# Kernel tuning notes

Measured on AMD Instinct MI355X. Metric: run time of the kernel, lower is better.

The kernel has to match this reference:

```python
import jax, jax.numpy as jnp
import numpy as np

V, E, H, L, B = 50000, 300, 128, 32, 8


def setup_inputs() -> dict:
    key = jax.random.key(0)
    ks = jax.random.split(key, 12)
    s = 0.05
    d = {}
    d["premise"] = jax.random.randint(ks[0], (B, L), 0, V)
    d["hypothesis"] = jax.random.randint(ks[1], (B, L), 0, V)
    d["emb"] = jax.random.normal(ks[2], (V, E), jnp.float32) * s
    d["W_ih"] = jax.random.normal(ks[3], (8 * H, 2 * E), jnp.float32) * s
    d["b_ih"] = jnp.zeros((8 * H,), jnp.float32)
    d["W_hh"] = jax.random.normal(ks[4], (8 * H, 2 * H), jnp.float32) * s
    d["b_hh"] = jnp.zeros((8 * H,), jnp.float32)
    d["W_ch"] = jax.random.normal(ks[5], (H, 2 * H), jnp.float32) * s
    d["b_ch"] = jnp.zeros((H,), jnp.float32)
    d["W_cc"] = jax.random.normal(ks[6], (H, 2 * H), jnp.float32) * s
    d["b_cc"] = jnp.zeros((H,), jnp.float32)
    d["W1"] = jax.random.normal(ks[7], (H, H), jnp.float32) * s
    d["b1"] = jnp.zeros((H,), jnp.float32)
    d["W2"] = jax.random.normal(ks[8], (H, H), jnp.float32) * s
    d["b2"] = jnp.zeros((H,), jnp.float32)
    d["W3"] = jax.random.normal(ks[9], (3, H), jnp.float32) * s
    d["b3"] = jnp.zeros((3,), jnp.float32)
    return d


def _lstm_cell(x, h, c, W_ih, b_ih, W_hh, b_hh):
    # PyTorch LSTMCell gate order: i, f, g, o
    g = x @ W_ih.T + b_ih + h @ W_hh.T + b_hh
    i, f, gg, o = jnp.split(g, 4, axis=-1)
    c_new = jax.nn.sigmoid(f) * c + jax.nn.sigmoid(i) * jnp.tanh(gg)
    h_new = jax.nn.sigmoid(o) * jnp.tanh(c_new)
    return h_new, c_new


def reference(premise, hypothesis, emb, W_ih, b_ih, W_hh, b_hh,
              W_ch, b_ch, W_cc, b_cc, W1, b1, W2, b2, W3, b3):
    p = emb[premise]      # [B, L, E]
    hyp = emb[hypothesis]  # [B, L, E]
    Bn, Ln, En = p.shape
    Hn = W_ch.shape[0]
    p_t = jnp.swapaxes(p, 0, 1)    # [L, B, E]
    hyp_t = jnp.swapaxes(hyp, 0, 1)
    z = jnp.zeros((Bn, Hn), p.dtype)

    def row_step(row_carry, p_i):
        h_up, c_up = row_carry  # [L, B, H] from previous row (left deps)

        def col_step(carry, xs):
            h_low, c_low = carry       # [B, H] from previous column (lower deps)
            h_u, c_u, x_hyp = xs       # [B,H], [B,H], [B,E]
            x = jnp.concatenate([p_i, x_hyp], axis=-1)       # [B, 2E]
            h_in = jnp.concatenate([h_u, h_low], axis=-1)    # left then lower -> [B, 2H]
            c_in = jnp.concatenate([c_u, c_low], axis=-1)
            h_o, c_o = _lstm_cell(x, h_in, c_in, W_ih, b_ih, W_hh, b_hh)
            h_n = h_o @ W_ch.T + b_ch  # condense back to [B, H]
            c_n = c_o @ W_cc.T + b_cc
            return (h_n, c_n), (h_n, c_n)

        _, (h_row, c_row) = jax.lax.scan(col_step, (z, z), (h_up, c_up, hyp_t))
        return (h_row, c_row), None

    init = (jnp.zeros((Ln, Bn, Hn), p.dtype), jnp.zeros((Ln, Bn, Hn), p.dtype))
    (h_grid, _), _ = jax.lax.scan(row_step, init, p_t)
    h = h_grid[-1]  # h[L, L] corner state, [B, H]
    h = jax.nn.relu(h @ W1.T + b1)
    h = jax.nn.relu(h @ W2.T + b2)
    return jax.nn.softmax(h @ W3.T + b3, axis=1)
```

## Files before the change

### kernel.cpp

```cpp
#include <hip/hip_runtime.h>
#include <math.h>


typedef _Float16 h2 __attribute__((ext_vector_type(2)));

__device__ __forceinline__ h2 pk_f16(float a, float b) {
    return __builtin_bit_cast(h2, __builtin_amdgcn_cvt_pkrtz(a, b));
}

#define HYP_OFF   0
#define HO_OFF    262144
#define CO_OFF    524288
#define WP_OFF    786432
#define B_OFF     1048576
#define FLAGS_OFF 1050624

#define BASE 0xAAAAAAAAu

__device__ __forceinline__ float sigm(float x) { return 1.f / (1.f + __expf(-x)); }
__device__ __forceinline__ float tanh_fast(float x) { return 1.f - 2.f / (__expf(2.f * x) + 1.f); }

__device__ __forceinline__ unsigned ld_flag(const unsigned* p) {
    return __hip_atomic_load(p, __ATOMIC_RELAXED, __HIP_MEMORY_SCOPE_AGENT);
}
__device__ __forceinline__ void st_flag(unsigned* p, unsigned v) {
    __hip_atomic_store(p, v, __ATOMIC_RELAXED, __HIP_MEMORY_SCOPE_AGENT);
}
__device__ __forceinline__ float ld_f32(const float* p) {
    unsigned u = __hip_atomic_load((const unsigned*)p, __ATOMIC_RELAXED, __HIP_MEMORY_SCOPE_AGENT);
    return __uint_as_float(u);
}
__device__ __forceinline__ void st_f32(float* p, float v) {
    __hip_atomic_store((unsigned*)p, __float_as_uint(v), __ATOMIC_RELAXED, __HIP_MEMORY_SCOPE_AGENT);
}
__device__ __forceinline__ void st_u32(unsigned* p, unsigned v) {
    __hip_atomic_store(p, v, __ATOMIC_RELAXED, __HIP_MEMORY_SCOPE_AGENT);
}
__device__ __forceinline__ float2 ld_f32x2(const float* p) {
    unsigned long long u = __hip_atomic_load((const unsigned long long*)p,
                                             __ATOMIC_RELAXED, __HIP_MEMORY_SCOPE_AGENT);
    float2 r; r.x = __uint_as_float((unsigned)u); r.y = __uint_as_float((unsigned)(u >> 32));
    return r;
}
__device__ __forceinline__ void ld_u32x2(const unsigned* p, unsigned& a, unsigned& b) {
    unsigned long long u = __hip_atomic_load((const unsigned long long*)p,
                                             __ATOMIC_RELAXED, __HIP_MEMORY_SCOPE_AGENT);
    a = (unsigned)u; b = (unsigned)(u >> 32);
}
__device__ __forceinline__ void wait_ge(const unsigned* f, unsigned target) {
    long spins = 0;
    while ((ld_flag(f) - BASE) < target) {
        __builtin_amdgcn_s_sleep(1);
        if (++spins > (1L << 22)) break;
    }
}
__device__ __forceinline__ void drain_vmem() {
    asm volatile("s_waitcnt vmcnt(0)" ::: "memory");
}

__global__ void __launch_bounds__(256, 1) grid_lstm_kernel(
    const int* __restrict__ premise, const int* __restrict__ hypothesis,
    const float* __restrict__ emb,
    const float* __restrict__ W_ih, const float* __restrict__ b_ih,
    const float* __restrict__ W_hh, const float* __restrict__ b_hh,
    const float* __restrict__ W_ch, const float* __restrict__ b_ch,
    const float* __restrict__ W_cc, const float* __restrict__ b_cc,
    const float* __restrict__ W1, const float* __restrict__ b1,
    const float* __restrict__ W2, const float* __restrict__ b2,
    const float* __restrict__ W3, const float* __restrict__ b3,
    float* __restrict__ out, float* __restrict__ ws)
{
    __shared__ h2    hAB[2048];
    __shared__ float sCo[2048];
    __shared__ float ppL[1024];
    __shared__ float red[8448];
    __shared__ float red2[2304];

    const int tid = threadIdx.x;
    const int bid = blockIdx.x;
    const int i   = bid & 31;
    const int c   = bid >> 5;

    float*    Hypproj = ws + HYP_OFF;
    float*    Ho      = ws + HO_OFF;
    float*    Co      = ws + CO_OFF;
    unsigned* WP      = (unsigned*)(ws + WP_OFF);
    float*    BU      = ws + B_OFF;
    float*    BL      = ws + B_OFF + 1024;
    unsigned* HF      = (unsigned*)(ws + FLAGS_OFF);
    unsigned* InitF   = (unsigned*)(ws + FLAGS_OFF) + 4096;

    const int tq = tid & 31, ks = tid >> 5;
    const int tl = tid & 31, bb = tid >> 5;

    {
        float* embs = red;
        for (int idx = tid; idx < 4800; idx += 256) {
            int side = idx / 2400, rem = idx - side * 2400;
            int b = rem / 300, e = rem - b * 300;
            const int* toks = side ? hypothesis : premise;
            embs[idx] = emb[(long)toks[b * 32 + i] * 300 + e];
        }
        __syncthreads();
        #pragma unroll 1
        for (int q = 0; q < 4; q++) {
            const int oo = tid + q * 256;
            const int b = oo >> 7, g = oo & 127;
            const int gr = (g >> 5) * 256 + c * 32 + (g & 31);
            float accP = b_ih[gr] + b_hh[gr];
            float accH = 0.f;
            const float* wp = W_ih + (long)gr * 600;
            const float* eP = embs + b * 300;
            const float* eH = embs + 2400 + b * 300;
            for (int e = 0; e < 300; e += 4) {
                float4 w1 = *(const float4*)(wp + e);
                float4 w2v = *(const float4*)(wp + 300 + e);
                float4 p4 = *(const float4*)(eP + e);
                float4 h4 = *(const float4*)(eH + e);
                accP += w1.x * p4.x + w1.y * p4.y + w1.z * p4.z + w1.w * p4.w;
                accH += w2v.x * h4.x + w2v.y * h4.y + w2v.z * h4.z + w2v.w * h4.w;
            }
            st_f32(&Hypproj[i * 8192 + b * 1024 + gr], accH);
            ppL[b * 128 + g] = accP;
        }
        __syncthreads();
    }

    {
        const int tr = tid >> 6, col = (tid & 63) * 4;
        const int r  = bid * 4 + tr;
        float u[4] = {0.f, 0.f, 0.f, 0.f}, l[4] = {0.f, 0.f, 0.f, 0.f};
        const float* whU = W_hh + (long)r * 256;
        const float* whL = whU + 128;
        for (int k = 0; k < 128; k++) {
            const float wu = whU[k], wl = whL[k];
            float4 wc = *(const float4*)(W_ch + (long)k * 256 + col);
            u[0] += wu * wc.x; u[1] += wu * wc.y; u[2] += wu * wc.z; u[3] += wu * wc.w;
            l[0] += wl * wc.x; l[1] += wl * wc.y; l[2] += wl * wc.z; l[3] += wl * wc.w;
        }
        unsigned* wrow = WP + (long)r * 256;
        st_u32(&wrow[col / 2],       __builtin_bit_cast(unsigned, __builtin_amdgcn_cvt_pkrtz(u[0], u[1])));
        st_u32(&wrow[col / 2 + 1],   __builtin_bit_cast(unsigned, __builtin_amdgcn_cvt_pkrtz(u[2], u[3])));
        st_u32(&wrow[128 + col / 2],     __builtin_bit_cast(unsigned, __builtin_amdgcn_cvt_pkrtz(l[0], l[1])));
        st_u32(&wrow[128 + col / 2 + 1], __builtin_bit_cast(unsigned, __builtin_amdgcn_cvt_pkrtz(l[2], l[3])));
        if ((tid & 63) == 0) {
            float su = 0.f, sl = 0.f;
            for (int k = 0; k < 128; k++) { su += whU[k] * b_ch[k]; sl += whL[k] * b_ch[k]; }
            st_f32(&BU[r], su); st_f32(&BL[r], sl);
        }
    }
    drain_vmem();
    __syncthreads();
    if (tid == 0) st_flag(&InitF[bid * 16], BASE + 1u);

    wait_ge(&InitF[tid * 16], 1u);
    __syncthreads();

    h2 w[4][32];
    #pragma unroll
    for (int a = 0; a < 4; a++) {
        const unsigned* src = WP + (long)(a * 256 + c * 32 + tq) * 256 + ks * 32;
        #pragma unroll
        for (int m = 0; m < 16; m++) {
            unsigned lo, hi;
            ld_u32x2(src + m * 2, lo, hi);
            w[a][2 * m]     = __builtin_bit_cast(h2, lo);
            w[a][2 * m + 1] = __builtin_bit_cast(h2, hi);
        }
    }
    float4 w3[8];
    {
        const float* wr = W_cc + (long)((c & 3) * 32 + tq) * 256 + ks * 32;
        #pragma unroll
        for (int m = 0; m < 8; m++) w3[m] = *(const float4*)(wr + m * 4);
    }
    float bUv[4], bLv[4];
    #pragma unroll
    for (int a = 0; a < 4; a++) {
        bUv[a] = ld_f32(&BU[a * 256 + c * 32 + tl]);
        bLv[a] = ld_f32(&BL[a * 256 + c * 32 + tl]);
    }

    #pragma unroll 1
    for (int j = 0; j < 32; j++) {
        const bool upok = (i > 0), lfok = (j > 0);
        const bool cok  = (c < 4) ? upok : lfok;
        const int  jl   = lfok ? (j - 1) : 0;

        if (upok && tid < 8)              wait_ge(&HF[((i - 1) * 8 + tid) * 16], (unsigned)(j + 1));
        if (lfok && tid >= 8 && tid < 16) wait_ge(&HF[(i * 8 + (tid - 8)) * 16], (unsigned)j);
        __syncthreads();

        float hyv[4];
        #pragma unroll
        for (int a = 0; a < 4; a++)
            hyv[a] = ld_f32(&Hypproj[j * 8192 + bb * 1024 + a * 256 + c * 32 + tl]);

        const float* HoUp = Ho + ((((i - 1) & 3) * 32 + j) * 2048);
        const float* HoLf = Ho + (((i & 3) * 32 + jl) * 2048);
        const float* CoS  = (c < 4) ? Co + ((((i - 1) & 3) * 32 + j) * 2048)
                                    : Co + (((i & 3) * 32 + jl) * 2048);
        #pragma unroll
        for (int r = 0; r < 4; r++) {
            const int idx = r * 256 + tid;
            const int b = idx >> 7, kk = idx & 127;
            float2 u = upok ? ld_f32x2(HoUp + b * 256 + 2 * kk) : make_float2(0.f, 0.f);
            float2 l = lfok ? ld_f32x2(HoLf + b * 256 + 2 * kk) : make_float2(0.f, 0.f);
            float2 cv = cok ? ld_f32x2(CoS + b * 256 + 2 * kk) : make_float2(0.f, 0.f);
            hAB[b * 256 + kk]       = pk_f16(u.x, u.y);
            hAB[b * 256 + 128 + kk] = pk_f16(l.x, l.y);
            sCo[b * 256 + 2 * kk] = cv.x; sCo[b * 256 + 2 * kk + 1] = cv.y;
        }
        __syncthreads();

        float acc[4][8], a3[8];
        #pragma unroll
        for (int a = 0; a < 4; a++)
            #pragma unroll
            for (int b = 0; b < 8; b++) acc[a][b] = 0.f;
        #pragma unroll
        for (int b = 0; b < 8; b++) a3[b] = 0.f;
        #pragma unroll
        for (int b = 0; b < 8; b++) {
            const h2*    hb = hAB + b * 256 + ks * 32;
            const float* cb = sCo + b * 256 + ks * 32;
            #pragma unroll
            for (int m4 = 0; m4 < 8; m4++) {
                uint4 hu = *(const uint4*)(hb + m4 * 4);
                h2 h0 = __builtin_bit_cast(h2, hu.x);
                h2 h1 = __builtin_bit_cast(h2, hu.y);
                h2 h2v = __builtin_bit_cast(h2, hu.z);
                h2 h3 = __builtin_bit_cast(h2, hu.w);
                #pragma unroll
                for (int a = 0; a < 4; a++) {
                    acc[a][b] = __builtin_amdgcn_fdot2(w[a][m4 * 4],     h0,  acc[a][b], false);
                    acc[a][b] = __builtin_amdgcn_fdot2(w[a][m4 * 4 + 1], h1,  acc[a][b], false);
                    acc[a][b] = __builtin_amdgcn_fdot2(w[a][m4 * 4 + 2], h2v, acc[a][b], false);
                    acc[a][b] = __builtin_amdgcn_fdot2(w[a][m4 * 4 + 3], h3,  acc[a][b], false);
                }
                float4 cv = *(const float4*)(cb + m4 * 4);
                a3[b] += w3[m4].x * cv.x + w3[m4].y * cv.y + w3[m4].z * cv.z + w3[m4].w * cv.w;
            }
        }
        #pragma unroll
        for (int a = 0; a < 4; a++)
            #pragma unroll
            for (int b = 0; b < 8; b++) red[tid * 33 + a * 8 + b] = acc[a][b];
        #pragma unroll
        for (int b = 0; b < 8; b++) red2[tid * 9 + b] = a3[b];
        __syncthreads();

        {
            float g4[4];
            #pragma unroll
            for (int a = 0; a < 4; a++) {
                float s = 0.f;
                #pragma unroll
                for (int k = 0; k < 8; k++)
                    s += red[(k * 32 + tl) * 33 + a * 8 + bb];
                s += ppL[bb * 128 + a * 32 + tl] + hyv[a];
                if (upok) s += bUv[a];
                if (lfok) s += bLv[a];
                g4[a] = s;
            }
            float ci = 0.f;
            #pragma unroll
            for (int k = 0; k < 8; k++) ci += red2[(k * 32 + tl) * 9 + bb];
            if (cok) ci += b_cc[(c & 3) * 32 + tl];
            const float cnew = sigm(g4[1]) * ci + sigm(g4[0]) * tanh_fast(g4[2]);
            const float hnew = sigm(g4[3]) * tanh_fast(cnew);
            const int base = ((i & 3) * 32 + j) * 2048 + bb * 256 + c * 32 + tl;
            st_f32(&Ho[base], hnew);
            st_f32(&Co[base], cnew);
        }
        drain_vmem();
        __syncthreads();
        if (tid == 0) st_flag(&HF[(i * 8 + c) * 16], BASE + (unsigned)(j + 1));
    }

    if (bid == 31) {
        if (tid < 8) wait_ge(&HF[(31 * 8 + tid) * 16], 32u);
        __syncthreads();
        const float* HoF = Ho + (((31 & 3) * 32 + 31) * 2048);
        #pragma unroll
        for (int r = 0; r < 4; r++) {
            const int idx = r * 256 + tid;
            float2 v = ld_f32x2(HoF + idx * 2);
            sCo[idx * 2] = v.x; sCo[idx * 2 + 1] = v.y;
        }
        __syncthreads();
        #pragma unroll 1
        for (int q = 0; q < 4; q++) {
            const int oo = tid + q * 256;
            const int b = oo >> 7, o = oo & 127;
            float a = b_ch[o];
            const float* wr = W_ch + (long)o * 256;
            const float* x = sCo + b * 256;
            for (int k = 0; k < 256; k += 4) {
                float4 wv = *(const float4*)(wr + k);
                float4 xv = *(const float4*)(x + k);
                a += wv.x * xv.x + wv.y * xv.y + wv.z * xv.z + wv.w * xv.w;
            }
            ppL[b * 128 + o] = a;
        }
        __syncthreads();
        float* m1 = red;
        float* m2 = red + 1024;
        for (int idx = tid; idx < 1024; idx += 256) {
            int b = idx >> 7, o = idx & 127;
            float a = b1[o];
            const float* wr = W1 + o * 128; const float* x = ppL + b * 128;
            for (int k = 0; k < 128; k++) a += wr[k] * x[k];
            m1[idx] = fmaxf(a, 0.f);
        }
        __syncthreads();
        for (int idx = tid; idx < 1024; idx += 256) {
            int b = idx >> 7, o = idx & 127;
            float a = b2[o];
            const float* wr = W2 + o * 128; const float* x = m1 + b * 128;
            for (int k = 0; k < 128; k++) a += wr[k] * x[k];
            m2[idx] = fmaxf(a, 0.f);
        }
        __syncthreads();
        if (tid < 8) {
            const int b = tid;
            float lg[3];
            for (int cc = 0; cc < 3; cc++) {
                float a = b3[cc];
                const float* wr = W3 + cc * 128; const float* x = m2 + b * 128;
                for (int k = 0; k < 128; k++) a += wr[k] * x[k];
                lg[cc] = a;
            }
            float m = fmaxf(lg[0], fmaxf(lg[1], lg[2]));
            float e0 = expf(lg[0] - m), e1 = expf(lg[1] - m), e2 = expf(lg[2] - m);
            float s = e0 + e1 + e2;
            out[b * 3 + 0] = e0 / s;
            out[b * 3 + 1] = e1 / s;
            out[b * 3 + 2] = e2 / s;
        }
    }
}

extern "C" void kernel_launch(void* const* d_in, const int* in_sizes, int n_in,
                              void* d_out, int out_size, void* d_ws, size_t ws_size,
                              hipStream_t stream) {
    const int*   premise    = (const int*)d_in[0];
    const int*   hypothesis = (const int*)d_in[1];
    const float* emb        = (const float*)d_in[2];
    const float* W_ih       = (const float*)d_in[3];
    const float* b_ih       = (const float*)d_in[4];
    const float* W_hh       = (const float*)d_in[5];
    const float* b_hh       = (const float*)d_in[6];
    const float* W_ch       = (const float*)d_in[7];
    const float* b_ch       = (const float*)d_in[8];
    const float* W_cc       = (const float*)d_in[9];
    const float* b_cc       = (const float*)d_in[10];
    const float* W1         = (const float*)d_in[11];
    const float* b1         = (const float*)d_in[12];
    const float* W2         = (const float*)d_in[13];
    const float* b2         = (const float*)d_in[14];
    const float* W3         = (const float*)d_in[15];
    const float* b3         = (const float*)d_in[16];
    float* out = (float*)d_out;
    float* ws  = (float*)d_ws;

    (void)in_sizes; (void)n_in; (void)out_size; (void)ws_size;

    grid_lstm_kernel<<<dim3(256), dim3(256), 0, stream>>>(
        premise, hypothesis, emb, W_ih, b_ih, W_hh, b_hh,
        W_ch, b_ch, W_cc, b_cc, W1, b1, W2, b2, W3, b3, out, ws);
}
```

Baseline: 815.9 us.

## Split recurrent matvec so left-dependency half runs before waiting on upper row

The per-step wait on both the upper-row and left-column flags is split into two phases. The block first waits only on its own row's previous column, loads the left h/c state and computes the left half of the recurrent dot products. Only then does it wait for the upper row's flag and compute the upper half. This overlaps computation with the cross-block dependency wait in the wavefront. It adds an extra barrier and reshuffles the weight register layout.

```diff
diff --git a/kernel.cpp b/kernel.cpp
--- a/kernel.cpp
+++ b/kernel.cpp
@@ -156,16 +156,20 @@
     wait_ge(&InitF[tid * 16], 1u);
     __syncthreads();
 
-    h2 w[4][32];
+    h2 w_u[4][16], w_l[4][16];
     #pragma unroll
     for (int a = 0; a < 4; a++) {
-        const unsigned* src = WP + (long)(a * 256 + c * 32 + tq) * 256 + ks * 32;
-        #pragma unroll
-        for (int m = 0; m < 16; m++) {
+        const unsigned* srcU = WP + (long)(a * 256 + c * 32 + tq) * 256 + ks * 16;
+        const unsigned* srcL = srcU + 128;
+        #pragma unroll
+        for (int m = 0; m < 8; m++) {
             unsigned lo, hi;
-            ld_u32x2(src + m * 2, lo, hi);
-            w[a][2 * m]     = __builtin_bit_cast(h2, lo);
-            w[a][2 * m + 1] = __builtin_bit_cast(h2, hi);
+            ld_u32x2(srcU + m * 2, lo, hi);
+            w_u[a][2 * m]     = __builtin_bit_cast(h2, lo);
+            w_u[a][2 * m + 1] = __builtin_bit_cast(h2, hi);
+            ld_u32x2(srcL + m * 2, lo, hi);
+            w_l[a][2 * m]     = __builtin_bit_cast(h2, lo);
+            w_l[a][2 * m + 1] = __builtin_bit_cast(h2, hi);
         }
     }
     float4 w3[8];
@@ -187,8 +191,7 @@
         const bool cok  = (c < 4) ? upok : lfok;
         const int  jl   = lfok ? (j - 1) : 0;
 
-        if (upok && tid < 8)              wait_ge(&HF[((i - 1) * 8 + tid) * 16], (unsigned)(j + 1));
-        if (lfok && tid >= 8 && tid < 16) wait_ge(&HF[(i * 8 + (tid - 8)) * 16], (unsigned)j);
+        if (lfok && tid < 8) wait_ge(&HF[(i * 8 + tid) * 16], (unsigned)j);
         __syncthreads();
 
         float hyv[4];
@@ -196,20 +199,18 @@
         for (int a = 0; a < 4; a++)
             hyv[a] = ld_f32(&Hypproj[j * 8192 + bb * 1024 + a * 256 + c * 32 + tl]);
 
-        const float* HoUp = Ho + ((((i - 1) & 3) * 32 + j) * 2048);
         const float* HoLf = Ho + (((i & 3) * 32 + jl) * 2048);
-        const float* CoS  = (c < 4) ? Co + ((((i - 1) & 3) * 32 + j) * 2048)
-                                    : Co + (((i & 3) * 32 + jl) * 2048);
+        const float* CoLf = Co + (((i & 3) * 32 + jl) * 2048);
         #pragma unroll
         for (int r = 0; r < 4; r++) {
             const int idx = r * 256 + tid;
             const int b = idx >> 7, kk = idx & 127;
-            float2 u = upok ? ld_f32x2(HoUp + b * 256 + 2 * kk) : make_float2(0.f, 0.f);
             float2 l = lfok ? ld_f32x2(HoLf + b * 256 + 2 * kk) : make_float2(0.f, 0.f);
-            float2 cv = cok ? ld_f32x2(CoS + b * 256 + 2 * kk) : make_float2(0.f, 0.f);
-            hAB[b * 256 + kk]       = pk_f16(u.x, u.y);
             hAB[b * 256 + 128 + kk] = pk_f16(l.x, l.y);
-            sCo[b * 256 + 2 * kk] = cv.x; sCo[b * 256 + 2 * kk + 1] = cv.y;
+            if (c >= 4) {
+                float2 cv = lfok ? ld_f32x2(CoLf + b * 256 + 2 * kk) : make_float2(0.f, 0.f);
+                sCo[b * 256 + 2 * kk] = cv.x; sCo[b * 256 + 2 * kk + 1] = cv.y;
+            }
         }
         __syncthreads();
 
@@ -222,10 +223,9 @@
         for (int b = 0; b < 8; b++) a3[b] = 0.f;
         #pragma unroll
         for (int b = 0; b < 8; b++) {
-            const h2*    hb = hAB + b * 256 + ks * 32;
-            const float* cb = sCo + b * 256 + ks * 32;
-            #pragma unroll
-            for (int m4 = 0; m4 < 8; m4++) {
+            const h2* hb = hAB + b * 256 + 128 + ks * 16;
+            #pragma unroll
+            for (int m4 = 0; m4 < 4; m4++) {
                 uint4 hu = *(const uint4*)(hb + m4 * 4);
                 h2 h0 = __builtin_bit_cast(h2, hu.x);
                 h2 h1 = __builtin_bit_cast(h2, hu.y);
@@ -233,13 +233,65 @@
                 h2 h3 = __builtin_bit_cast(h2, hu.w);
                 #pragma unroll
                 for (int a = 0; a < 4; a++) {
-                    acc[a][b] = __builtin_amdgcn_fdot2(w[a][m4 * 4],     h0,  acc[a][b], false);
-                    acc[a][b] = __builtin_amdgcn_fdot2(w[a][m4 * 4 + 1], h1,  acc[a][b], false);
-                    acc[a][b] = __builtin_amdgcn_fdot2(w[a][m4 * 4 + 2], h2v, acc[a][b], false);
-                    acc[a][b] = __builtin_amdgcn_fdot2(w[a][m4 * 4 + 3], h3,  acc[a][b], false);
+                    acc[a][b] = __builtin_amdgcn_fdot2(w_l[a][m4 * 4],     h0,  acc[a][b], false);
+                    acc[a][b] = __builtin_amdgcn_fdot2(w_l[a][m4 * 4 + 1], h1,  acc[a][b], false);
+                    acc[a][b] = __builtin_amdgcn_fdot2(w_l[a][m4 * 4 + 2], h2v, acc[a][b], false);
+                    acc[a][b] = __builtin_amdgcn_fdot2(w_l[a][m4 * 4 + 3], h3,  acc[a][b], false);
                 }
-                float4 cv = *(const float4*)(cb + m4 * 4);
-                a3[b] += w3[m4].x * cv.x + w3[m4].y * cv.y + w3[m4].z * cv.z + w3[m4].w * cv.w;
+            }
+            if (c >= 4) {
+                const float* cb = sCo + b * 256 + ks * 32;
+                #pragma unroll
+                for (int m = 0; m < 8; m++) {
+                    float4 cv = *(const float4*)(cb + m * 4);
+                    a3[b] += w3[m].x * cv.x + w3[m].y * cv.y + w3[m].z * cv.z + w3[m].w * cv.w;
+                }
+            }
+        }
+
+        if (upok && tid < 8) wait_ge(&HF[((i - 1) * 8 + tid) * 16], (unsigned)(j + 1));
+        __syncthreads();
+
+        const float* HoUp = Ho + ((((i - 1) & 3) * 32 + j) * 2048);
+        const float* CoUp = Co + ((((i - 1) & 3) * 32 + j) * 2048);
+        #pragma unroll
+        for (int r = 0; r < 4; r++) {
+            const int idx = r * 256 + tid;
+            const int b = idx >> 7, kk = idx & 127;
+            float2 u = upok ? ld_f32x2(HoUp + b * 256 + 2 * kk) : make_float2(0.f, 0.f);
+            hAB[b * 256 + kk] = pk_f16(u.x, u.y);
+            if (c < 4) {
+                float2 cv = upok ? ld_f32x2(CoUp + b * 256 + 2 * kk) : make_float2(0.f, 0.f);
+                sCo[b * 256 + 2 * kk] = cv.x; sCo[b * 256 + 2 * kk + 1] = cv.y;
+            }
+        }
+        __syncthreads();
+
+        #pragma unroll
+        for (int b = 0; b < 8; b++) {
+            const h2* hb = hAB + b * 256 + ks * 16;
+            #pragma unroll
+            for (int m4 = 0; m4 < 4; m4++) {
+                uint4 hu = *(const uint4*)(hb + m4 * 4);
+                h2 h0 = __builtin_bit_cast(h2, hu.x);
+                h2 h1 = __builtin_bit_cast(h2, hu.y);
+                h2 h2v = __builtin_bit_cast(h2, hu.z);
+                h2 h3 = __builtin_bit_cast(h2, hu.w);
+                #pragma unroll
+                for (int a = 0; a < 4; a++) {
+                    acc[a][b] = __builtin_amdgcn_fdot2(w_u[a][m4 * 4],     h0,  acc[a][b], false);
+                    acc[a][b] = __builtin_amdgcn_fdot2(w_u[a][m4 * 4 + 1], h1,  acc[a][b], false);
+                    acc[a][b] = __builtin_amdgcn_fdot2(w_u[a][m4 * 4 + 2], h2v, acc[a][b], false);
+                    acc[a][b] = __builtin_amdgcn_fdot2(w_u[a][m4 * 4 + 3], h3,  acc[a][b], false);
+                }
+            }
+            if (c < 4) {
+                const float* cb = sCo + b * 256 + ks * 32;
+                #pragma unroll
+                for (int m = 0; m < 8; m++) {
+                    float4 cv = *(const float4*)(cb + m * 4);
+                    a3[b] += w3[m].x * cv.x + w3[m].y * cv.y + w3[m].z * cv.z + w3[m].w * cv.w;
+                }
             }
         }
         #pragma unroll
```

New measurement: 913.6 us. +12.0%, slower.
